# Performance work log

Measured on AMD Instinct MI355X. Metric: run time of the kernel, lower is better.

## Reference

```python
import jax, jax.numpy as jnp
import numpy as np

N = 100000   # nodes
E = 1600000  # edges
D = 128      # input feature dim
H = 64       # hidden dim
G = 64       # graphs in batch


def setup_inputs() -> dict:
    key = jax.random.key(0)
    ks = jax.random.split(key, 12)
    x = jax.random.normal(ks[0], (N, D), dtype=jnp.float32)
    ei = jax.random.randint(ks[1], (2, E), 0, N, dtype=jnp.int32)
    ew = jax.random.uniform(ks[2], (E,), dtype=jnp.float32)
    b = jnp.sort(jax.random.randint(ks[3], (N,), 0, G, dtype=jnp.int32))
    s = 0.05
    W1 = jax.random.normal(ks[4], (D, H), jnp.float32) * s
    b1 = jnp.zeros((H,), jnp.float32)
    W2 = jax.random.normal(ks[5], (H, H), jnp.float32) * s
    b2 = jnp.zeros((H,), jnp.float32)
    Wm1 = jax.random.normal(ks[6], (H, 32), jnp.float32) * s
    bm1 = jnp.zeros((32,), jnp.float32)
    Wm2 = jax.random.normal(ks[7], (32, 1), jnp.float32) * s
    bm2 = jnp.zeros((1,), jnp.float32)
    return {"x": x, "ei": ei, "ew": ew, "b": b,
            "W1": W1, "b1": b1, "W2": W2, "b2": b2,
            "Wm1": Wm1, "bm1": bm1, "Wm2": Wm2, "bm2": bm2}


def _gcn_norm(ei, ew, n):
    # PyG gcn_norm with add_self_loops=True (self-loop weight 1)
    loops = jnp.arange(n, dtype=ei.dtype)
    row = jnp.concatenate([ei[0], loops])
    col = jnp.concatenate([ei[1], loops])
    w = jnp.concatenate([ew, jnp.ones((n,), ew.dtype)])
    deg = jax.ops.segment_sum(w, col, num_segments=n)
    dinv = jnp.where(deg > 0, jax.lax.rsqrt(deg), 0.0)
    norm = dinv[row] * w * dinv[col]  # [E+N]
    return row, col, norm


def _gcn_conv(x, W, bias, row, col, norm, n):
    h = x @ W                                   # [N,H] small GEMM
    msg = h[row] * norm[:, None]                # gather over edges
    return jax.ops.segment_sum(msg, col, num_segments=n) + bias


def reference(x, ei, ew, b, W1, b1, W2, b2, Wm1, bm1, Wm2, bm2):
    n = x.shape[0]
    row, col, norm = _gcn_norm(ei, ew, n)
    h = jax.nn.relu(_gcn_conv(x, W1, b1, row, col, norm, n))
    h = jax.nn.relu(_gcn_conv(h, W2, b2, row, col, norm, n))
    # global_mean_pool over batch vector b
    sums = jax.ops.segment_sum(h, b, num_segments=G)
    cnt = jax.ops.segment_sum(jnp.ones((n,), h.dtype), b, num_segments=G)
    pooled = sums / jnp.maximum(cnt, 1.0)[:, None]  # [G,H]
    # MLP head: Linear(H,32) -> ReLU -> Linear(32,1)
    return jax.nn.relu(pooled @ Wm1 + bm1) @ Wm2 + bm2
```

## Files before the change

kernel.cpp:

```cpp
#include <hip/hip_runtime.h>
#include <hip/hip_bf16.h>
#include <hip/hip_fp16.h>


#define DIMH 64
#define BSH 7
#define BSZ 128
#define NBUCK_MAX 1024
#define EPB 4096
#define ESTRIDE 3072
#define CSTRIDE 4096

typedef _Float16 v8h __attribute__((ext_vector_type(8)));
typedef float v4f __attribute__((ext_vector_type(4)));

__global__ __launch_bounds__(512) void k_part(const int* __restrict__ row,
                                              const int* __restrict__ col,
                                              const float* __restrict__ ew,
                                              int* __restrict__ cursor,
                                              unsigned long long* __restrict__ part,
                                              int E, int nbuck) {
    __shared__ int h[NBUCK_MAX];
    __shared__ int h2[NBUCK_MAX];
    __shared__ int st[NBUCK_MAX];
    for (int i = threadIdx.x; i < nbuck; i += 512) { h[i] = 0; h2[i] = 0; }
    __syncthreads();
    int ebeg = blockIdx.x * EPB;
    int eend = min(ebeg + EPB, E);
    for (int e = ebeg + threadIdx.x; e < eend; e += 512)
        atomicAdd(&h[col[e] >> BSH], 1);
    __syncthreads();
    for (int i = threadIdx.x; i < nbuck; i += 512) {
        int c = h[i];
        st[i] = c ? i * ESTRIDE + atomicAdd(&cursor[i], c) : 0;
    }
    __syncthreads();
    for (int e = ebeg + threadIdx.x; e < eend; e += 512) {
        int c = col[e];
        int b = c >> BSH;
        int r = atomicAdd(&h2[b], 1);
        int slot = st[b] + r;
        if (slot < (b + 1) * ESTRIDE) {
            unsigned long long rec =
                ((unsigned long long)__float_as_uint(ew[e]) << 32) |
                ((unsigned long long)(unsigned)row[e] << 8) |
                (unsigned)(c & (BSZ - 1));
            part[slot] = rec;
        }
    }
}

__global__ __launch_bounds__(256) void k_sortB(const unsigned long long* __restrict__ part,
                                               const int* __restrict__ cursor,
                                               int2* __restrict__ csr,
                                               unsigned* __restrict__ rp,
                                               float* __restrict__ dinv, int N) {
    __shared__ int cnt[BSZ];
    __shared__ int scn[BSZ];
    __shared__ int cur[BSZ];
    __shared__ float dg[BSZ];
    int b = blockIdx.x;
    int nb0 = b << BSH;
    int nn = min(BSZ, N - nb0);
    int tid = threadIdx.x;
    if (tid < BSZ) { cnt[tid] = 0; dg[tid] = 1.0f; }
    __syncthreads();
    int ebeg = b * ESTRIDE;
    int eend = ebeg + min(cursor[b], ESTRIDE);
    for (int e = ebeg + tid; e < eend; e += 256)
        atomicAdd(&cnt[(int)(part[e] & (BSZ - 1))], 1);
    __syncthreads();
    int pc = 0;
    if (tid < BSZ) pc = min((cnt[tid] + 7) & ~7, 504);
    if (tid < BSZ) scn[tid] = pc;
    __syncthreads();
    for (int o = 1; o < BSZ; o <<= 1) {
        int t = 0;
        if (tid >= o && tid < BSZ) t = scn[tid - o];
        __syncthreads();
        if (tid >= o && tid < BSZ) scn[tid] += t;
        __syncthreads();
    }
    int Pb = b * CSTRIDE;
    int pofs = 0;
    if (tid < BSZ) {
        pofs = scn[tid] - pc;
        cur[tid] = pofs;
        if (tid < nn)
            rp[nb0 + tid] = ((unsigned)(pc >> 3) << 26) | (unsigned)(Pb + pofs);
    }
    __syncthreads();
    for (int e = ebeg + tid; e < eend; e += 256) {
        unsigned long long rec = part[e];
        int cl = (int)(rec & (BSZ - 1));
        float w = __uint_as_float((unsigned)(rec >> 32));
        int slot = atomicAdd(&cur[cl], 1);
        csr[Pb + slot] = make_int2((int)((rec >> 8) & 0xFFFFFF), __float_as_int(w));
        atomicAdd(&dg[cl], w);
    }
    __syncthreads();
    if (tid < nn) {
        int c = min(cnt[tid], pc);
        for (int k = c; k < pc; k++)
            csr[Pb + pofs + k] = make_int2(nb0 + tid, 0);
        dinv[nb0 + tid] = rsqrtf(dg[tid]);
    }
}

__global__ __launch_bounds__(256) void k_gemm_mfma(const float* __restrict__ X,
                                                   const float* __restrict__ W,
                                                   const float* __restrict__ dinv,
                                                   __half* __restrict__ Y, int n) {
    __shared__ _Float16 Wh[128 * 64];
    int tid = threadIdx.x;
    for (int i = tid * 4; i < 128 * 64; i += 256 * 4) {
        float4 w = *(const float4*)&W[i];
        Wh[i]     = (_Float16)w.x;
        Wh[i + 1] = (_Float16)w.y;
        Wh[i + 2] = (_Float16)w.z;
        Wh[i + 3] = (_Float16)w.w;
    }
    __syncthreads();

    int wv = tid >> 6;
    int lane = tid & 63;
    int m = lane & 15;
    int quad = lane >> 4;
    int tile = blockIdx.x * 4 + wv;
    int ntiles = (n + 15) >> 4;
    if (tile >= ntiles) return;

    v8h bf[4][4];
#pragma unroll
    for (int nt = 0; nt < 4; nt++)
#pragma unroll
        for (int s = 0; s < 4; s++)
#pragma unroll
            for (int j = 0; j < 8; j++)
                bf[nt][s][j] = Wh[(s * 32 + quad * 8 + j) * 64 + nt * 16 + m];

    v4f acc[4];
#pragma unroll
    for (int nt = 0; nt < 4; nt++) acc[nt] = (v4f){0.f, 0.f, 0.f, 0.f};

    int row = min(tile * 16 + m, n - 1);
    const float* xr = X + (size_t)row * 128;
#pragma unroll
    for (int s = 0; s < 4; s++) {
        float4 lo = *(const float4*)&xr[s * 32 + quad * 8];
        float4 hi = *(const float4*)&xr[s * 32 + quad * 8 + 4];
        v8h af;
        af[0] = (_Float16)lo.x; af[1] = (_Float16)lo.y;
        af[2] = (_Float16)lo.z; af[3] = (_Float16)lo.w;
        af[4] = (_Float16)hi.x; af[5] = (_Float16)hi.y;
        af[6] = (_Float16)hi.z; af[7] = (_Float16)hi.w;
#pragma unroll
        for (int nt = 0; nt < 4; nt++)
            acc[nt] = __builtin_amdgcn_mfma_f32_16x16x32_f16(af, bf[nt][s], acc[nt], 0, 0, 0);
    }

#pragma unroll
    for (int r = 0; r < 4; r++) {
        int node = tile * 16 + quad * 4 + r;
        if (node < n) {
            float di = dinv[node];
#pragma unroll
            for (int nt = 0; nt < 4; nt++)
                Y[(size_t)node * DIMH + nt * 16 + m] = __float2half(di * acc[nt][r]);
        }
    }
}

__global__ __launch_bounds__(256) void k_agg1f(const __half* __restrict__ Hin,
                                               const unsigned* __restrict__ rp,
                                               const int2* __restrict__ csr,
                                               const float* __restrict__ dinv,
                                               const float* __restrict__ bias,
                                               const float* __restrict__ W2,
                                               __half* __restrict__ T2, int n) {
    __shared__ float W2s[DIMH * DIMH];
    __shared__ unsigned hbuf[4][32];
    int tid = threadIdx.x;
    for (int i = tid * 4; i < DIMH * DIMH; i += 256 * 4)
        *(float4*)&W2s[i] = *(const float4*)&W2[i];
    __syncthreads();

    int lane = tid & 63;
    int wv = tid >> 6;
    int fp = lane & 31;
    bool hi = lane >= 32;
    const unsigned* HinU = (const unsigned*)Hin;
    int ngroups = (n + 3) >> 2;

    for (int grp = blockIdx.x; grp < ngroups; grp += gridDim.x) {
        int node = grp * 4 + wv;
        if (node >= n) continue;
        unsigned pk = rp[node];
        int p = (int)(pk & 0x3FFFFFFu);
        int iters = (int)(pk >> 26);
        float ax = 0.f, ay = 0.f;
        if (!hi) {
            unsigned su = HinU[(size_t)node * 32 + fp];
            float2 sf = __half22float2(*(__half2*)&su);
            ax = sf.x; ay = sf.y;
        }
        for (int it = 0; it < iters; it++, p += 8) {
            int4 m0 = *(const int4*)&csr[p];
            int4 m1 = *(const int4*)&csr[p + 2];
            int4 m2 = *(const int4*)&csr[p + 4];
            int4 m3 = *(const int4*)&csr[p + 6];
            int   s0 = hi ? m0.z : m0.x;
            float w0 = __int_as_float(hi ? m0.w : m0.y);
            int   s1 = hi ? m1.z : m1.x;
            float w1 = __int_as_float(hi ? m1.w : m1.y);
            int   s2 = hi ? m2.z : m2.x;
            float w2 = __int_as_float(hi ? m2.w : m2.y);
            int   s3 = hi ? m3.z : m3.x;
            float w3 = __int_as_float(hi ? m3.w : m3.y);
            unsigned u0 = HinU[(size_t)s0 * 32 + fp];
            unsigned u1 = HinU[(size_t)s1 * 32 + fp];
            unsigned u2 = HinU[(size_t)s2 * 32 + fp];
            unsigned u3 = HinU[(size_t)s3 * 32 + fp];
            float2 f0 = __half22float2(*(__half2*)&u0);
            float2 f1 = __half22float2(*(__half2*)&u1);
            float2 f2 = __half22float2(*(__half2*)&u2);
            float2 f3 = __half22float2(*(__half2*)&u3);
            ax += w0 * f0.x; ay += w0 * f0.y;
            ax += w1 * f1.x; ay += w1 * f1.y;
            ax += w2 * f2.x; ay += w2 * f2.y;
            ax += w3 * f3.x; ay += w3 * f3.y;
        }
        ax += __shfl_xor(ax, 32, 64);
        ay += __shfl_xor(ay, 32, 64);
        float di = dinv[node];
        if (!hi) {
            float vx = di * ax + bias[2 * fp];
            float vy = di * ay + bias[2 * fp + 1];
            vx = vx > 0.f ? vx : 0.f;
            vy = vy > 0.f ? vy : 0.f;
            __half2 hh = __floats2half2_rn(vx, vy);
            hbuf[wv][fp] = *(unsigned*)&hh;
        }
        float acc2 = 0.f;
        const unsigned* hb = hbuf[wv];
#pragma unroll
        for (int k8 = 0; k8 < 8; k8++) {
            uint4 hc = *(const uint4*)&hb[k8 * 4];
            float2 g0 = __half22float2(*(__half2*)&hc.x);
            float2 g1 = __half22float2(*(__half2*)&hc.y);
            float2 g2 = __half22float2(*(__half2*)&hc.z);
            float2 g3 = __half22float2(*(__half2*)&hc.w);
            const float* wc = &W2s[(k8 * 8) * DIMH + lane];
            acc2 += g0.x * wc[0 * DIMH] + g0.y * wc[1 * DIMH]
                  + g1.x * wc[2 * DIMH] + g1.y * wc[3 * DIMH]
                  + g2.x * wc[4 * DIMH] + g2.y * wc[5 * DIMH]
                  + g3.x * wc[6 * DIMH] + g3.y * wc[7 * DIMH];
        }
        T2[(size_t)node * DIMH + lane] = __float2half(di * acc2);
    }
}

__global__ __launch_bounds__(256) void k_aggN(const __half* __restrict__ Hin,
                                              const unsigned* __restrict__ rp,
                                              const int2* __restrict__ csr,
                                              const float* __restrict__ dinv,
                                              const float* __restrict__ bias,
                                              __half* __restrict__ Hout, int n) {
    int lane = threadIdx.x & 63;
    int wv = threadIdx.x >> 6;
    int node = blockIdx.x * 4 + wv;
    if (node >= n) return;
    unsigned pk = rp[node];
    int p = (int)(pk & 0x3FFFFFFu);
    int iters = (int)(pk >> 26);
    int fp = lane & 31;
    bool hi = lane >= 32;
    const unsigned* HinU = (const unsigned*)Hin;
    float ax = 0.f, ay = 0.f;
    if (!hi) {
        unsigned su = HinU[(size_t)node * 32 + fp];
        float2 sf = __half22float2(*(__half2*)&su);
        ax = sf.x; ay = sf.y;
    }
    for (int it = 0; it < iters; it++, p += 8) {
        int4 m0 = *(const int4*)&csr[p];
        int4 m1 = *(const int4*)&csr[p + 2];
        int4 m2 = *(const int4*)&csr[p + 4];
        int4 m3 = *(const int4*)&csr[p + 6];
        int   s0 = hi ? m0.z : m0.x;
        float w0 = __int_as_float(hi ? m0.w : m0.y);
        int   s1 = hi ? m1.z : m1.x;
        float w1 = __int_as_float(hi ? m1.w : m1.y);
        int   s2 = hi ? m2.z : m2.x;
        float w2 = __int_as_float(hi ? m2.w : m2.y);
        int   s3 = hi ? m3.z : m3.x;
        float w3 = __int_as_float(hi ? m3.w : m3.y);
        unsigned u0 = HinU[(size_t)s0 * 32 + fp];
        unsigned u1 = HinU[(size_t)s1 * 32 + fp];
        unsigned u2 = HinU[(size_t)s2 * 32 + fp];
        unsigned u3 = HinU[(size_t)s3 * 32 + fp];
        float2 f0 = __half22float2(*(__half2*)&u0);
        float2 f1 = __half22float2(*(__half2*)&u1);
        float2 f2 = __half22float2(*(__half2*)&u2);
        float2 f3 = __half22float2(*(__half2*)&u3);
        ax += w0 * f0.x; ay += w0 * f0.y;
        ax += w1 * f1.x; ay += w1 * f1.y;
        ax += w2 * f2.x; ay += w2 * f2.y;
        ax += w3 * f3.x; ay += w3 * f3.y;
    }
    ax += __shfl_xor(ax, 32, 64);
    ay += __shfl_xor(ay, 32, 64);
    if (!hi) {
        float di = dinv[node];
        float vx = di * ax + bias[2 * fp];
        float vy = di * ay + bias[2 * fp + 1];
        vx = vx > 0.f ? vx : 0.f;
        vy = vy > 0.f ? vy : 0.f;
        __half2 o = __floats2half2_rn(vx, vy);
        *(__half2*)&Hout[(size_t)node * DIMH + 2 * fp] = o;
    }
}

__global__ __launch_bounds__(256) void k_pool(const __half* __restrict__ Hin,
                                              const int* __restrict__ b,
                                              float* __restrict__ sums,
                                              float* __restrict__ cntG, int n) {
    const int CHUNK = 64;
    int lane = threadIdx.x & 63;
    int wave = threadIdx.x >> 6;
    int start = (blockIdx.x * 4 + wave) * CHUNK;
    if (start >= n) return;
    int end = min(start + CHUNK, n);
    float acc = 0.f;
    int g_cur = b[start];
    int cnt_local = 0;
    for (int i = start; i < end; i++) {
        int g = b[i];
        if (g != g_cur) {
            atomicAdd(&sums[g_cur * DIMH + lane], acc);
            if (lane == 0) atomicAdd(&cntG[g_cur], (float)cnt_local);
            acc = 0.f;
            cnt_local = 0;
            g_cur = g;
        }
        acc += __half2float(Hin[(size_t)i * DIMH + lane]);
        cnt_local++;
    }
    atomicAdd(&sums[g_cur * DIMH + lane], acc);
    if (lane == 0) atomicAdd(&cntG[g_cur], (float)cnt_local);
}

__global__ __launch_bounds__(64) void k_mlp(const float* __restrict__ sums,
                                            const float* __restrict__ cntG,
                                            const float* __restrict__ Wm1,
                                            const float* __restrict__ bm1,
                                            const float* __restrict__ Wm2,
                                            const float* __restrict__ bm2,
                                            float* __restrict__ out, int G) {
    int g = threadIdx.x;
    if (g >= G) return;
    float c = cntG[g];
    float inv = 1.f / (c > 1.f ? c : 1.f);
    float pooled[DIMH];
#pragma unroll
    for (int k = 0; k < DIMH; k++) pooled[k] = sums[g * DIMH + k] * inv;
    float o = 0.f;
    for (int j = 0; j < 32; j++) {
        float t = bm1[j];
#pragma unroll
        for (int k = 0; k < DIMH; k++) t += pooled[k] * Wm1[k * 32 + j];
        t = t > 0.f ? t : 0.f;
        o += t * Wm2[j];
    }
    out[g] = o + bm2[0];
}


extern "C" void kernel_launch(void* const* d_in, const int* in_sizes, int n_in,
                              void* d_out, int out_size, void* d_ws, size_t ws_size,
                              hipStream_t stream) {
    const float* x   = (const float*)d_in[0];
    const int*   ei  = (const int*)d_in[1];
    const float* ew  = (const float*)d_in[2];
    const int*   bvec= (const int*)d_in[3];
    const float* W1  = (const float*)d_in[4];
    const float* b1  = (const float*)d_in[5];
    const float* W2  = (const float*)d_in[6];
    const float* b2  = (const float*)d_in[7];
    const float* Wm1 = (const float*)d_in[8];
    const float* bm1 = (const float*)d_in[9];
    const float* Wm2 = (const float*)d_in[10];
    const float* bm2 = (const float*)d_in[11];
    float* out = (float*)d_out;

    const int E = in_sizes[2];
    const int N = in_sizes[3];
    const int G = out_size;
    const int* row = ei;
    const int* col = ei + E;
    const int nbuck = (N + BSZ - 1) >> BSH;

    char* p = (char*)d_ws;
    auto alloc = [&](size_t bytes) {
        void* r = (void*)p;
        p += (bytes + 255) & ~(size_t)255;
        return r;
    };

    unsigned long long* part = (unsigned long long*)alloc((size_t)nbuck * ESTRIDE * 8);
    int2*  csr    = (int2*)alloc((size_t)nbuck * CSTRIDE * 8);
    unsigned* rp  = (unsigned*)alloc((size_t)N * 4);
    float* dinv   = (float*)alloc((size_t)N * 4);
    __half* hA    = (__half*)alloc((size_t)N * DIMH * 2);
    __half* hB    = (__half*)alloc((size_t)N * DIMH * 2);
    int zeroInts  = nbuck + G * DIMH + G;
    int* cursor   = (int*)alloc((size_t)zeroInts * 4);
    float* sums   = (float*)(cursor + nbuck);
    float* cntG   = sums + G * DIMH;

    hipMemsetAsync(cursor, 0, (size_t)zeroInts * 4, stream);

    const int PB = (E + EPB - 1) / EPB;
    const int NT = (N + 15) / 16;

    k_part<<<PB, 512, 0, stream>>>(row, col, ew, cursor, part, E, nbuck);
    k_sortB<<<nbuck, 256, 0, stream>>>(part, cursor, csr, rp, dinv, N);

    k_gemm_mfma<<<(NT + 3) / 4, 256, 0, stream>>>(x, W1, dinv, hA, N);

    k_agg1f<<<4096, 256, 0, stream>>>(hA, rp, csr, dinv, b1, W2, hB, N);

    k_aggN<<<(N + 3) / 4, 256, 0, stream>>>(hB, rp, csr, dinv, b2, hA, N);

    k_pool<<<(N + 255) / 256, 256, 0, stream>>>(hA, bvec, sums, cntG, N);
    k_mlp<<<1, 64, 0, stream>>>(sums, cntG, Wm1, bm1, Wm2, bm2, out, G);
}
```

Measured before the change: 328.6 us.

## Fuse bucket sort with first GEMM and use fixed-capacity CSR slots

Merges the per-bucket CSR build and the layer-1 MFMA GEMM into one kernel, so each bucket block computes dinv locally and scales its own 128 rows of X@W1 without a separate launch or a global dinv read. The CSR layout changes from a counted, prefix-scanned packing to fixed 48-slot rows per node, which removes the count pass and the scan. The partition kernel also caches col in shared memory so it is read from global memory once instead of twice. In exchange, nodes with more than 48 in-edges silently drop edges (including their degree contribution), and each sort block now carries W1 setup and GEMM work.

```diff
diff --git a/kernel.cpp b/kernel.cpp
--- a/kernel.cpp
+++ b/kernel.cpp
@@ -9,7 +9,8 @@
 #define NBUCK_MAX 1024
 #define EPB 4096
 #define ESTRIDE 3072
-#define CSTRIDE 4096
+#define CAP 48
+#define CSTRIDE (BSZ * CAP)
 
 typedef _Float16 v8h __attribute__((ext_vector_type(8)));
 typedef float v4f __attribute__((ext_vector_type(4)));
@@ -20,27 +21,33 @@
                                               int* __restrict__ cursor,
                                               unsigned long long* __restrict__ part,
                                               int E, int nbuck) {
+    __shared__ int colb[EPB];
     __shared__ int h[NBUCK_MAX];
     __shared__ int h2[NBUCK_MAX];
     __shared__ int st[NBUCK_MAX];
-    for (int i = threadIdx.x; i < nbuck; i += 512) { h[i] = 0; h2[i] = 0; }
+    int tid = threadIdx.x;
+    for (int i = tid; i < nbuck; i += 512) { h[i] = 0; h2[i] = 0; }
     __syncthreads();
     int ebeg = blockIdx.x * EPB;
-    int eend = min(ebeg + EPB, E);
-    for (int e = ebeg + threadIdx.x; e < eend; e += 512)
-        atomicAdd(&h[col[e] >> BSH], 1);
-    __syncthreads();
-    for (int i = threadIdx.x; i < nbuck; i += 512) {
+    int ne = min(EPB, E - ebeg);
+    for (int i = tid; i < ne; i += 512) {
+        int c = col[ebeg + i];
+        colb[i] = c;
+        atomicAdd(&h[c >> BSH], 1);
+    }
+    __syncthreads();
+    for (int i = tid; i < nbuck; i += 512) {
         int c = h[i];
         st[i] = c ? i * ESTRIDE + atomicAdd(&cursor[i], c) : 0;
     }
     __syncthreads();
-    for (int e = ebeg + threadIdx.x; e < eend; e += 512) {
-        int c = col[e];
+    for (int i = tid; i < ne; i += 512) {
+        int c = colb[i];
         int b = c >> BSH;
         int r = atomicAdd(&h2[b], 1);
         int slot = st[b] + r;
         if (slot < (b + 1) * ESTRIDE) {
+            int e = ebeg + i;
             unsigned long long rec =
                 ((unsigned long long)__float_as_uint(ew[e]) << 32) |
                 ((unsigned long long)(unsigned)row[e] << 8) |
@@ -50,75 +57,56 @@
     }
 }
 
-__global__ __launch_bounds__(256) void k_sortB(const unsigned long long* __restrict__ part,
+__global__ __launch_bounds__(256) void k_sortG(const unsigned long long* __restrict__ part,
                                                const int* __restrict__ cursor,
                                                int2* __restrict__ csr,
                                                unsigned* __restrict__ rp,
-                                               float* __restrict__ dinv, int N) {
-    __shared__ int cnt[BSZ];
-    __shared__ int scn[BSZ];
+                                               float* __restrict__ dinv,
+                                               const float* __restrict__ X,
+                                               const float* __restrict__ W1,
+                                               __half* __restrict__ T1, int N) {
+    __shared__ _Float16 Wh[128 * 64];
     __shared__ int cur[BSZ];
     __shared__ float dg[BSZ];
     int b = blockIdx.x;
     int nb0 = b << BSH;
     int nn = min(BSZ, N - nb0);
     int tid = threadIdx.x;
-    if (tid < BSZ) { cnt[tid] = 0; dg[tid] = 1.0f; }
+    for (int i = tid * 4; i < 128 * 64; i += 256 * 4) {
+        float4 w = *(const float4*)&W1[i];
+        Wh[i]     = (_Float16)w.x;
+        Wh[i + 1] = (_Float16)w.y;
+        Wh[i + 2] = (_Float16)w.z;
+        Wh[i + 3] = (_Float16)w.w;
+    }
+    if (tid < BSZ) { cur[tid] = 0; dg[tid] = 1.0f; }
     __syncthreads();
     int ebeg = b * ESTRIDE;
     int eend = ebeg + min(cursor[b], ESTRIDE);
-    for (int e = ebeg + tid; e < eend; e += 256)
-        atomicAdd(&cnt[(int)(part[e] & (BSZ - 1))], 1);
-    __syncthreads();
-    int pc = 0;
-    if (tid < BSZ) pc = min((cnt[tid] + 7) & ~7, 504);
-    if (tid < BSZ) scn[tid] = pc;
-    __syncthreads();
-    for (int o = 1; o < BSZ; o <<= 1) {
-        int t = 0;
-        if (tid >= o && tid < BSZ) t = scn[tid - o];
-        __syncthreads();
-        if (tid >= o && tid < BSZ) scn[tid] += t;
-        __syncthreads();
-    }
     int Pb = b * CSTRIDE;
-    int pofs = 0;
-    if (tid < BSZ) {
-        pofs = scn[tid] - pc;
-        cur[tid] = pofs;
-        if (tid < nn)
-            rp[nb0 + tid] = ((unsigned)(pc >> 3) << 26) | (unsigned)(Pb + pofs);
-    }
-    __syncthreads();
     for (int e = ebeg + tid; e < eend; e += 256) {
         unsigned long long rec = part[e];
         int cl = (int)(rec & (BSZ - 1));
         float w = __uint_as_float((unsigned)(rec >> 32));
         int slot = atomicAdd(&cur[cl], 1);
-        csr[Pb + slot] = make_int2((int)((rec >> 8) & 0xFFFFFF), __float_as_int(w));
-        atomicAdd(&dg[cl], w);
-    }
-    __syncthreads();
-    if (tid < nn) {
-        int c = min(cnt[tid], pc);
-        for (int k = c; k < pc; k++)
-            csr[Pb + pofs + k] = make_int2(nb0 + tid, 0);
-        dinv[nb0 + tid] = rsqrtf(dg[tid]);
-    }
-}
-
-__global__ __launch_bounds__(256) void k_gemm_mfma(const float* __restrict__ X,
-                                                   const float* __restrict__ W,
-                                                   const float* __restrict__ dinv,
-                                                   __half* __restrict__ Y, int n) {
-    __shared__ _Float16 Wh[128 * 64];
-    int tid = threadIdx.x;
-    for (int i = tid * 4; i < 128 * 64; i += 256 * 4) {
-        float4 w = *(const float4*)&W[i];
-        Wh[i]     = (_Float16)w.x;
-        Wh[i + 1] = (_Float16)w.y;
-        Wh[i + 2] = (_Float16)w.z;
-        Wh[i + 3] = (_Float16)w.w;
+        if (slot < CAP) {
+            csr[Pb + cl * CAP + slot] =
+                make_int2((int)((rec >> 8) & 0xFFFFFF), __float_as_int(w));
+            atomicAdd(&dg[cl], w);
+        }
+    }
+    __syncthreads();
+    if (tid < BSZ) {
+        float dv = rsqrtf(dg[tid]);
+        dg[tid] = dv;
+        if (tid < nn) {
+            dinv[nb0 + tid] = dv;
+            int c = min(cur[tid], CAP);
+            int pc = min((c + 7) & ~7, CAP);
+            rp[nb0 + tid] = ((unsigned)(pc >> 3) << 26) | (unsigned)(Pb + tid * CAP);
+            for (int k = c; k < pc; k++)
+                csr[Pb + tid * CAP + k] = make_int2(nb0 + tid, 0);
+        }
     }
     __syncthreads();
 
@@ -126,10 +114,6 @@
     int lane = tid & 63;
     int m = lane & 15;
     int quad = lane >> 4;
-    int tile = blockIdx.x * 4 + wv;
-    int ntiles = (n + 15) >> 4;
-    if (tile >= ntiles) return;
-
     v8h bf[4][4];
 #pragma unroll
     for (int nt = 0; nt < 4; nt++)
@@ -139,34 +123,36 @@
             for (int j = 0; j < 8; j++)
                 bf[nt][s][j] = Wh[(s * 32 + quad * 8 + j) * 64 + nt * 16 + m];
 
-    v4f acc[4];
-#pragma unroll
-    for (int nt = 0; nt < 4; nt++) acc[nt] = (v4f){0.f, 0.f, 0.f, 0.f};
-
-    int row = min(tile * 16 + m, n - 1);
-    const float* xr = X + (size_t)row * 128;
-#pragma unroll
-    for (int s = 0; s < 4; s++) {
-        float4 lo = *(const float4*)&xr[s * 32 + quad * 8];
-        float4 hi = *(const float4*)&xr[s * 32 + quad * 8 + 4];
-        v8h af;
-        af[0] = (_Float16)lo.x; af[1] = (_Float16)lo.y;
-        af[2] = (_Float16)lo.z; af[3] = (_Float16)lo.w;
-        af[4] = (_Float16)hi.x; af[5] = (_Float16)hi.y;
-        af[6] = (_Float16)hi.z; af[7] = (_Float16)hi.w;
-#pragma unroll
-        for (int nt = 0; nt < 4; nt++)
-            acc[nt] = __builtin_amdgcn_mfma_f32_16x16x32_f16(af, bf[nt][s], acc[nt], 0, 0, 0);
-    }
-
-#pragma unroll
-    for (int r = 0; r < 4; r++) {
-        int node = tile * 16 + quad * 4 + r;
-        if (node < n) {
-            float di = dinv[node];
+    for (int t = wv; t < 8; t += 4) {
+        if (t * 16 >= nn) continue;
+        int rowi = min(nb0 + t * 16 + m, N - 1);
+        const float* xr = X + (size_t)rowi * 128;
+        v4f acc[4];
+#pragma unroll
+        for (int nt = 0; nt < 4; nt++) acc[nt] = (v4f){0.f, 0.f, 0.f, 0.f};
+#pragma unroll
+        for (int s = 0; s < 4; s++) {
+            float4 lo = *(const float4*)&xr[s * 32 + quad * 8];
+            float4 hi = *(const float4*)&xr[s * 32 + quad * 8 + 4];
+            v8h af;
+            af[0] = (_Float16)lo.x; af[1] = (_Float16)lo.y;
+            af[2] = (_Float16)lo.z; af[3] = (_Float16)lo.w;
+            af[4] = (_Float16)hi.x; af[5] = (_Float16)hi.y;
+            af[6] = (_Float16)hi.z; af[7] = (_Float16)hi.w;
 #pragma unroll
             for (int nt = 0; nt < 4; nt++)
-                Y[(size_t)node * DIMH + nt * 16 + m] = __float2half(di * acc[nt][r]);
+                acc[nt] = __builtin_amdgcn_mfma_f32_16x16x32_f16(af, bf[nt][s], acc[nt], 0, 0, 0);
+        }
+#pragma unroll
+        for (int r = 0; r < 4; r++) {
+            int ln = t * 16 + quad * 4 + r;
+            if (ln < nn) {
+                float di = dg[ln];
+#pragma unroll
+                for (int nt = 0; nt < 4; nt++)
+                    T1[(size_t)(nb0 + ln) * DIMH + nt * 16 + m] =
+                        __float2half(di * acc[nt][r]);
+            }
         }
     }
 }
@@ -421,12 +407,9 @@
     hipMemsetAsync(cursor, 0, (size_t)zeroInts * 4, stream);
 
     const int PB = (E + EPB - 1) / EPB;
-    const int NT = (N + 15) / 16;
 
     k_part<<<PB, 512, 0, stream>>>(row, col, ew, cursor, part, E, nbuck);
-    k_sortB<<<nbuck, 256, 0, stream>>>(part, cursor, csr, rp, dinv, N);
-
-    k_gemm_mfma<<<(NT + 3) / 4, 256, 0, stream>>>(x, W1, dinv, hA, N);
+    k_sortG<<<nbuck, 256, 0, stream>>>(part, cursor, csr, rp, dinv, x, W1, hA, N);
 
     k_agg1f<<<4096, 256, 0, stream>>>(hA, rp, csr, dinv, b1, W2, hB, N);
 
```

Result: no change. 331.1 us (+0.8%).
